# Kernel tuning notes

Measured on AMD Instinct MI355X. Metric: run time of the kernel, lower is better.

Reference implementation:

```python
import jax, jax.numpy as jnp
import numpy as np

REP_THR = 0.6
BORDER = 10


def setup_inputs() -> dict:
    key = jax.random.key(0)
    repeatability = jax.random.uniform(key, (8, 1, 2048, 2048), dtype=jnp.float32)
    return {"repeatability": repeatability}


def reference(repeatability):
    # 3x3 max pool, stride 1, pad 1 (torch pads with -inf for max pool)
    local_max = jax.lax.reduce_window(
        repeatability,
        -jnp.inf,
        jax.lax.max,
        window_dimensions=(1, 1, 3, 3),
        window_strides=(1, 1, 1, 1),
        padding=[(0, 0), (0, 0), (1, 1), (1, 1)],
    )
    maxima = (repeatability == local_max) & (repeatability >= REP_THR)
    # border mask: zero out a 10-pixel frame
    B, C, H, W = repeatability.shape
    border = jnp.zeros((H, W), dtype=bool).at[BORDER:-BORDER, BORDER:-BORDER].set(True)
    maxima = maxima & border  # broadcast over (B, C)
    # Original returns maxima.nonzero().t()[2:4] (data-dependent shape);
    # for jit-compatibility we return the dense boolean mask as float32 —
    # the (y, x) indices are exactly the nonzero positions of this mask.
    return maxima.astype(jnp.float32)
```

## Files before the change

kernel.cpp:

```cpp
#include <hip/hip_runtime.h>
#include <math.h>

#define IMG_H 2048
#define IMG_W 2048
#define NB    8
#define BORDER 10
#define REP_THR 0.6f

__global__ __launch_bounds__(256) void nms_kernel(const float* __restrict__ in,
                                                  float* __restrict__ out) {
    const int tid = blockIdx.x * blockDim.x + threadIdx.x;
    const int gx = tid & 511;
    const int gy = (tid >> 9) & 511;
    const int b  = tid >> 18;

    const int x4 = gx << 2;
    const int y0 = gy << 2;

    const size_t img_off = (size_t)b * IMG_H * IMG_W;
    float* obase = out + img_off + (size_t)y0 * IMG_W + x4;

    if (y0 + 4 <= BORDER || y0 >= IMG_H - BORDER || gx == 0 || gx == 511) {
        const float4 z = make_float4(0.f, 0.f, 0.f, 0.f);
        *(float4*)(obase + 0 * IMG_W) = z;
        *(float4*)(obase + 1 * IMG_W) = z;
        *(float4*)(obase + 2 * IMG_W) = z;
        *(float4*)(obase + 3 * IMG_W) = z;
        return;
    }

    const float* base = in + img_off + (size_t)(y0 - 1) * IMG_W + x4;

    float4 h[6];
    float4 c[4];
#pragma unroll
    for (int r = 0; r < 6; ++r) {
        const float* row = base + (size_t)r * IMG_W;
        const float4 v = *(const float4*)row;
        const float  l = row[-1];
        const float  q = row[4];
        float4 hh;
        hh.x = fmaxf(l,   fmaxf(v.x, v.y));
        hh.y = fmaxf(v.x, fmaxf(v.y, v.z));
        hh.z = fmaxf(v.y, fmaxf(v.z, v.w));
        hh.w = fmaxf(v.z, fmaxf(v.w, q));
        h[r] = hh;
        if (r >= 1 && r <= 4) c[r - 1] = v;
    }

    const bool bx0 = (x4 + 0 >= BORDER) && (x4 + 0 < IMG_W - BORDER);
    const bool bx1 = (x4 + 1 >= BORDER) && (x4 + 1 < IMG_W - BORDER);
    const bool bx2 = (x4 + 2 >= BORDER) && (x4 + 2 < IMG_W - BORDER);
    const bool bx3 = (x4 + 3 >= BORDER) && (x4 + 3 < IMG_W - BORDER);

#pragma unroll
    for (int j = 0; j < 4; ++j) {
        const int y = y0 + j;
        const bool rowok = (y >= BORDER) && (y < IMG_H - BORDER);

        float4 m;
        m.x = fmaxf(h[j].x, fmaxf(h[j + 1].x, h[j + 2].x));
        m.y = fmaxf(h[j].y, fmaxf(h[j + 1].y, h[j + 2].y));
        m.z = fmaxf(h[j].z, fmaxf(h[j + 1].z, h[j + 2].z));
        m.w = fmaxf(h[j].w, fmaxf(h[j + 1].w, h[j + 2].w));

        float4 r;
        r.x = (c[j].x == m.x && c[j].x >= REP_THR && bx0 && rowok) ? 1.f : 0.f;
        r.y = (c[j].y == m.y && c[j].y >= REP_THR && bx1 && rowok) ? 1.f : 0.f;
        r.z = (c[j].z == m.z && c[j].z >= REP_THR && bx2 && rowok) ? 1.f : 0.f;
        r.w = (c[j].w == m.w && c[j].w >= REP_THR && bx3 && rowok) ? 1.f : 0.f;

        *(float4*)(obase + (size_t)j * IMG_W) = r;
    }
}

extern "C" void kernel_launch(void* const* d_in, const int* in_sizes, int n_in,
                              void* d_out, int out_size, void* d_ws, size_t ws_size,
                              hipStream_t stream) {
    const float* in = (const float*)d_in[0];
    float* out = (float*)d_out;
    const int total_threads = NB * (IMG_H / 4) * (IMG_W / 4);
    const int block = 256;
    const int grid = total_threads / block;
    nms_kernel<<<grid, block, 0, stream>>>(in, out);
}
```

Baseline: 226.5 us.

## Process 16 rows per thread with a rolling row window and nontemporal stores

```diff
diff --git a/kernel.cpp b/kernel.cpp
--- a/kernel.cpp
+++ b/kernel.cpp
@@ -6,71 +6,84 @@
 #define NB    8
 #define BORDER 10
 #define REP_THR 0.6f
+#define RPT   16
+
+
+typedef float vfloat4 __attribute__((ext_vector_type(4)));
+
+__device__ __forceinline__ void nt_store4(float* p, float a, float b, float c, float d) {
+    vfloat4 v = {a, b, c, d};
+    __builtin_nontemporal_store(v, (vfloat4*)p);
+}
+
+struct RowH { float4 v; float4 h; };
+
+__device__ __forceinline__ RowH load_row(const float* __restrict__ row) {
+    RowH r;
+    r.v = *(const float4*)row;
+    const float l = row[-1];
+    const float q = row[4];
+    r.h.x = fmaxf(l,     fmaxf(r.v.x, r.v.y));
+    r.h.y = fmaxf(r.v.x, fmaxf(r.v.y, r.v.z));
+    r.h.z = fmaxf(r.v.y, fmaxf(r.v.z, r.v.w));
+    r.h.w = fmaxf(r.v.z, fmaxf(r.v.w, q));
+    return r;
+}
 
 __global__ __launch_bounds__(256) void nms_kernel(const float* __restrict__ in,
                                                   float* __restrict__ out) {
     const int tid = blockIdx.x * blockDim.x + threadIdx.x;
     const int gx = tid & 511;
-    const int gy = (tid >> 9) & 511;
-    const int b  = tid >> 18;
+    const int s  = (tid >> 9) & 127;
+    const int b  = tid >> 16;
 
     const int x4 = gx << 2;
-    const int y0 = gy << 2;
+    const int y0 = s * RPT;
 
     const size_t img_off = (size_t)b * IMG_H * IMG_W;
     float* obase = out + img_off + (size_t)y0 * IMG_W + x4;
 
-    if (y0 + 4 <= BORDER || y0 >= IMG_H - BORDER || gx == 0 || gx == 511) {
-        const float4 z = make_float4(0.f, 0.f, 0.f, 0.f);
-        *(float4*)(obase + 0 * IMG_W) = z;
-        *(float4*)(obase + 1 * IMG_W) = z;
-        *(float4*)(obase + 2 * IMG_W) = z;
-        *(float4*)(obase + 3 * IMG_W) = z;
+    if (gx == 0 || gx == 511) {
+#pragma unroll
+        for (int j = 0; j < RPT; ++j)
+            nt_store4(obase + (size_t)j * IMG_W, 0.f, 0.f, 0.f, 0.f);
         return;
     }
 
-    const float* base = in + img_off + (size_t)(y0 - 1) * IMG_W + x4;
-
-    float4 h[6];
-    float4 c[4];
-#pragma unroll
-    for (int r = 0; r < 6; ++r) {
-        const float* row = base + (size_t)r * IMG_W;
-        const float4 v = *(const float4*)row;
-        const float  l = row[-1];
-        const float  q = row[4];
-        float4 hh;
-        hh.x = fmaxf(l,   fmaxf(v.x, v.y));
-        hh.y = fmaxf(v.x, fmaxf(v.y, v.z));
-        hh.z = fmaxf(v.y, fmaxf(v.z, v.w));
-        hh.w = fmaxf(v.z, fmaxf(v.w, q));
-        h[r] = hh;
-        if (r >= 1 && r <= 4) c[r - 1] = v;
-    }
+    const float* ibase = in + img_off + x4;
 
     const bool bx0 = (x4 + 0 >= BORDER) && (x4 + 0 < IMG_W - BORDER);
     const bool bx1 = (x4 + 1 >= BORDER) && (x4 + 1 < IMG_W - BORDER);
     const bool bx2 = (x4 + 2 >= BORDER) && (x4 + 2 < IMG_W - BORDER);
     const bool bx3 = (x4 + 3 >= BORDER) && (x4 + 3 < IMG_W - BORDER);
 
+    const int ym = (y0 == 0) ? 0 : (y0 - 1);
+    RowH A = load_row(ibase + (size_t)ym * IMG_W);
+    RowH B = load_row(ibase + (size_t)y0 * IMG_W);
+
 #pragma unroll
-    for (int j = 0; j < 4; ++j) {
+    for (int j = 0; j < RPT; ++j) {
+        int yn = y0 + j + 1;
+        if (yn > IMG_H - 1) yn = IMG_H - 1;
+        const RowH C = load_row(ibase + (size_t)yn * IMG_W);
+
+        float4 m;
+        m.x = fmaxf(A.h.x, fmaxf(B.h.x, C.h.x));
+        m.y = fmaxf(A.h.y, fmaxf(B.h.y, C.h.y));
+        m.z = fmaxf(A.h.z, fmaxf(B.h.z, C.h.z));
+        m.w = fmaxf(A.h.w, fmaxf(B.h.w, C.h.w));
+
         const int y = y0 + j;
         const bool rowok = (y >= BORDER) && (y < IMG_H - BORDER);
 
-        float4 m;
-        m.x = fmaxf(h[j].x, fmaxf(h[j + 1].x, h[j + 2].x));
-        m.y = fmaxf(h[j].y, fmaxf(h[j + 1].y, h[j + 2].y));
-        m.z = fmaxf(h[j].z, fmaxf(h[j + 1].z, h[j + 2].z));
-        m.w = fmaxf(h[j].w, fmaxf(h[j + 1].w, h[j + 2].w));
+        const float r0 = (B.v.x == m.x && B.v.x >= REP_THR && bx0 && rowok) ? 1.f : 0.f;
+        const float r1 = (B.v.y == m.y && B.v.y >= REP_THR && bx1 && rowok) ? 1.f : 0.f;
+        const float r2 = (B.v.z == m.z && B.v.z >= REP_THR && bx2 && rowok) ? 1.f : 0.f;
+        const float r3 = (B.v.w == m.w && B.v.w >= REP_THR && bx3 && rowok) ? 1.f : 0.f;
 
-        float4 r;
-        r.x = (c[j].x == m.x && c[j].x >= REP_THR && bx0 && rowok) ? 1.f : 0.f;
-        r.y = (c[j].y == m.y && c[j].y >= REP_THR && bx1 && rowok) ? 1.f : 0.f;
-        r.z = (c[j].z == m.z && c[j].z >= REP_THR && bx2 && rowok) ? 1.f : 0.f;
-        r.w = (c[j].w == m.w && c[j].w >= REP_THR && bx3 && rowok) ? 1.f : 0.f;
+        nt_store4(obase + (size_t)j * IMG_W, r0, r1, r2, r3);
 
-        *(float4*)(obase + (size_t)j * IMG_W) = r;
+        A = B; B = C;
     }
 }
 
@@ -79,7 +92,7 @@
                               hipStream_t stream) {
     const float* in = (const float*)d_in[0];
     float* out = (float*)d_out;
-    const int total_threads = NB * (IMG_H / 4) * (IMG_W / 4);
+    const int total_threads = NB * (IMG_H / RPT) * (IMG_W / 4);
     const int block = 256;
     const int grid = total_threads / block;
     nms_kernel<<<grid, block, 0, stream>>>(in, out);
```

New measurement: 236.7 us. +4.5%, slower.
